# Kernel tuning notes

Measured on AMD Instinct MI355X. Metric: run time of the kernel, lower is better.

Reference implementation:

```python
import jax, jax.numpy as jnp
import numpy as np

N_NODES = 50000
N_EDGES = 800000
NEG_SLOPE = 0.2


def gat_conv(x, W, al, ar, b, src, dst, num_nodes):
    # x: [N, Din]; W: [Din, H*Dout]; al/ar: [H, Dout]; b: [H*Dout]
    H, Dout = al.shape
    h = (x @ W).reshape(num_nodes, H, Dout)            # [N, H, Dout]
    el = jnp.sum(h * al[None], axis=-1)                # [N, H]
    er = jnp.sum(h * ar[None], axis=-1)                # [N, H]
    e = jax.nn.leaky_relu(el[src] + er[dst], NEG_SLOPE)  # [E, H]
    # segment softmax over incoming edges of each dst node
    m = jax.ops.segment_max(e, dst, num_segments=num_nodes)
    m = jnp.where(jnp.isfinite(m), m, 0.0)
    ex = jnp.exp(e - m[dst])                           # [E, H]
    s = jax.ops.segment_sum(ex, dst, num_segments=num_nodes)
    alpha = ex / s[dst]                                # [E, H]
    msg = h[src] * alpha[:, :, None]                   # [E, H, Dout]
    out = jax.ops.segment_sum(msg, dst, num_segments=num_nodes)
    return out + b.reshape(1, H, Dout)                 # [N, H, Dout]


def setup_inputs() -> dict:
    key = jax.random.key(0)
    ks = jax.random.split(key, 12)
    d_in, hid, heads = 128, 128, 2
    inp = {
        "embedding": jax.random.normal(ks[0], (N_NODES, d_in), jnp.float32),
        "W0": jax.random.normal(ks[1], (d_in, heads * hid), jnp.float32) * 0.1,
        "al0": jax.random.normal(ks[2], (heads, hid), jnp.float32) * 0.1,
        "ar0": jax.random.normal(ks[3], (heads, hid), jnp.float32) * 0.1,
        "b0": jnp.zeros((heads * hid,), jnp.float32),
        "W1": jax.random.normal(ks[4], (heads * hid, heads * hid), jnp.float32) * 0.1,
        "al1": jax.random.normal(ks[5], (1, heads * hid), jnp.float32) * 0.1,
        "ar1": jax.random.normal(ks[6], (1, heads * hid), jnp.float32) * 0.1,
        "b1": jnp.zeros((heads * hid,), jnp.float32),
        "src": jax.random.randint(ks[7], (N_EDGES,), 0, N_NODES, jnp.int32),
        "dst": jax.random.randint(ks[8], (N_EDGES,), 0, N_NODES, jnp.int32),
    }
    return inp


def reference(embedding, W0, al0, ar0, b0, W1, al1, ar1, b1, src, dst):
    n = embedding.shape[0]
    # layer 0: 2 heads, then flatten heads and ReLU (dropout no-op in eval)
    x = gat_conv(embedding, W0, al0, ar0, b0, src, dst, n)  # [N, 2, 128]
    x = jax.nn.relu(x.reshape(n, -1))                        # [N, 256]
    # layer 1: 1 head, squeeze
    x = gat_conv(x, W1, al1, ar1, b1, src, dst, n)           # [N, 1, 256]
    x = x.reshape(n, -1)
    x = x.at[0].set(0.0)
    return x
```

## Files before the change

kernel.cpp:

```cpp
#include <hip/hip_runtime.h>


typedef __attribute__((ext_vector_type(8))) short short8v;
typedef __attribute__((ext_vector_type(4))) float f32x4;

#define LOG2E 1.4426950408889634f

__device__ inline unsigned short f2bf(float x) {
    union { float f; unsigned int u; } v; v.f = x;
    unsigned int r = v.u + 0x7fffu + ((v.u >> 16) & 1u);
    return (unsigned short)(r >> 16);
}
__device__ inline float bf2f(unsigned short h) {
    union { unsigned int u; float f; } v; v.u = ((unsigned int)h) << 16;
    return v.f;
}

__global__ void convW_both(const float* __restrict__ W0, unsigned short* __restrict__ W0t,
                           const float* __restrict__ W1, unsigned short* __restrict__ W1t)
{
    int t = blockIdx.x * blockDim.x + threadIdx.x;
    if (t < 128 * 256) {
        int k = t >> 8, n2 = t & 255;
        W0t[n2 * 128 + k] = f2bf(W0[t]);
    }
    int u = t - 128 * 256;
    if (u >= 0 && u < 256 * 256) {
        int k = u >> 8, n2 = u & 255;
        W1t[n2 * 256 + k] = f2bf(W1[u]);
    }
}

template<int AFP32, int H>
__global__ __launch_bounds__(256) void gemm_fused(
    const void* __restrict__ Av, const unsigned short* __restrict__ Bt,
    unsigned short* __restrict__ C,
    const float* __restrict__ al, const float* __restrict__ ar,
    float* __restrict__ el, float* __restrict__ er,
    int M, int N, int K)
{
    __shared__ __align__(16) unsigned short As[128 * 64];
    __shared__ __align__(16) unsigned short Bs[64 * 64];
    const int tid = threadIdx.x;
    const int lane = tid & 63, wv = tid >> 6;
    const int rowBase = blockIdx.x * 128;
    const int colBase = blockIdx.y * 64;

    f32x4 acc[2][4];
    #pragma unroll
    for (int i = 0; i < 2; ++i)
        #pragma unroll
        for (int j = 0; j < 4; ++j)
            acc[i][j] = (f32x4){0.f, 0.f, 0.f, 0.f};

    for (int k0 = 0; k0 < K; k0 += 64) {
        #pragma unroll
        for (int c = tid; c < 128 * 8; c += 256) {
            int row = c >> 3, cc = c & 7;
            int gr = rowBase + row; if (gr >= M) gr = M - 1;
            unsigned short* dstp = &As[row * 64 + (cc ^ (row & 7)) * 8];
            if (AFP32) {
                const float* A = (const float*)Av;
                const float* ap = A + (size_t)gr * K + k0 + cc * 8;
                float4 v0 = *(const float4*)ap;
                float4 v1 = *(const float4*)(ap + 4);
                ushort4 o0, o1;
                o0.x = f2bf(v0.x); o0.y = f2bf(v0.y); o0.z = f2bf(v0.z); o0.w = f2bf(v0.w);
                o1.x = f2bf(v1.x); o1.y = f2bf(v1.y); o1.z = f2bf(v1.z); o1.w = f2bf(v1.w);
                *(ushort4*)dstp = o0;
                *(ushort4*)(dstp + 4) = o1;
            } else {
                const unsigned short* A = (const unsigned short*)Av;
                int4 v = *(const int4*)(A + (size_t)gr * K + k0 + cc * 8);
                *(int4*)dstp = v;
            }
        }
        #pragma unroll
        for (int c = tid; c < 64 * 8; c += 256) {
            int n2 = c >> 3, cc = c & 7;
            int4 v = *(const int4*)(Bt + (size_t)(colBase + n2) * K + k0 + cc * 8);
            *(int4*)&Bs[n2 * 64 + (cc ^ (n2 & 7)) * 8] = v;
        }
        __syncthreads();

        #pragma unroll
        for (int ks = 0; ks < 64; ks += 32) {
            int kchunk = (ks >> 3) + (lane >> 4);
            short8v af[2], bfr[4];
            #pragma unroll
            for (int fm = 0; fm < 2; ++fm) {
                int ml = wv * 32 + fm * 16 + (lane & 15);
                af[fm] = *(const short8v*)&As[ml * 64 + (kchunk ^ (ml & 7)) * 8];
            }
            #pragma unroll
            for (int fi = 0; fi < 4; ++fi) {
                int nl = fi * 16 + (lane & 15);
                bfr[fi] = *(const short8v*)&Bs[nl * 64 + (kchunk ^ (nl & 7)) * 8];
            }
            #pragma unroll
            for (int fm = 0; fm < 2; ++fm)
                #pragma unroll
                for (int fi = 0; fi < 4; ++fi)
                    acc[fm][fi] = __builtin_amdgcn_mfma_f32_16x16x32_bf16(
                        af[fm], bfr[fi], acc[fm][fi], 0, 0, 0);
        }
        __syncthreads();
    }

    float alv[4], arv[4];
    #pragma unroll
    for (int fi = 0; fi < 4; ++fi) {
        int col = colBase + fi * 16 + (lane & 15);
        alv[fi] = al[col];
        arv[fi] = ar[col];
    }
    const int head = (H == 2) ? (colBase >> 7) : 0;

    #pragma unroll
    for (int fm = 0; fm < 2; ++fm) {
        #pragma unroll
        for (int r = 0; r < 4; ++r) {
            int row = rowBase + wv * 32 + fm * 16 + (lane >> 4) * 4 + r;
            float pe = acc[fm][0][r] * alv[0] + acc[fm][1][r] * alv[1]
                     + acc[fm][2][r] * alv[2] + acc[fm][3][r] * alv[3];
            float pr2 = acc[fm][0][r] * arv[0] + acc[fm][1][r] * arv[1]
                      + acc[fm][2][r] * arv[2] + acc[fm][3][r] * arv[3];
            #pragma unroll
            for (int off = 8; off; off >>= 1) {
                pe  += __shfl_xor(pe, off);
                pr2 += __shfl_xor(pr2, off);
            }
            if (row < M) {
                #pragma unroll
                for (int fi = 0; fi < 4; ++fi) {
                    int col = colBase + fi * 16 + (lane & 15);
                    C[(size_t)row * N + col] = f2bf(acc[fm][fi][r]);
                }
                if ((lane & 15) == 0) {
                    atomicAdd(&el[row * H + head], pe);
                    atomicAdd(&er[row * H + head], pr2);
                }
            }
        }
    }
}

__global__ void count_kernel(const int* __restrict__ dst, int* __restrict__ cnt, int E)
{
    int t = blockIdx.x * blockDim.x + threadIdx.x;
    if (t < E) atomicAdd(&cnt[dst[t]], 1);
}

__global__ __launch_bounds__(256) void scan_partial(const int* __restrict__ cnt,
                                                    int* __restrict__ bsum, int n)
{
    int t = threadIdx.x;
    int idx = blockIdx.x * 1024 + t * 4;
    int4 v = make_int4(0, 0, 0, 0);
    if (idx + 3 < n) v = *(const int4*)(cnt + idx);
    else if (idx < n) {
        v.x = cnt[idx];
        if (idx + 1 < n) v.y = cnt[idx + 1];
        if (idx + 2 < n) v.z = cnt[idx + 2];
    }
    int s = v.x + v.y + v.z + v.w;
    #pragma unroll
    for (int off = 32; off; off >>= 1) s += __shfl_xor(s, off);
    __shared__ int ws[4];
    if ((t & 63) == 0) ws[t >> 6] = s;
    __syncthreads();
    if (t == 0) bsum[blockIdx.x] = ws[0] + ws[1] + ws[2] + ws[3];
}

__global__ void scan_bsum(int* __restrict__ bsum, int* __restrict__ row,
                          int nb, int n, int E)
{
    int t = threadIdx.x;
    if (nb <= 64) {
        int v = (t < nb) ? bsum[t] : 0;
        int x = v;
        #pragma unroll
        for (int off = 1; off < 64; off <<= 1) {
            int y = __shfl_up(x, off);
            if (t >= off) x += y;
        }
        if (t < nb) bsum[t] = x - v;
    } else if (t == 0) {
        int run = 0;
        for (int i = 0; i < nb; ++i) { int v = bsum[i]; bsum[i] = run; run += v; }
    }
    if (t == 0) row[n] = E;
}

__global__ __launch_bounds__(256) void scan_final(
    const int* __restrict__ cnt, const int* __restrict__ bsum,
    int* __restrict__ row, int* __restrict__ cursor, int n)
{
    int t = threadIdx.x;
    int lane = t & 63;
    int idx = blockIdx.x * 1024 + t * 4;
    int4 v = make_int4(0, 0, 0, 0);
    if (idx + 3 < n) v = *(const int4*)(cnt + idx);
    else if (idx < n) {
        v.x = cnt[idx];
        if (idx + 1 < n) v.y = cnt[idx + 1];
        if (idx + 2 < n) v.z = cnt[idx + 2];
    }
    int s1 = v.x + v.y, s2 = s1 + v.z, s3 = s2 + v.w;
    int tsum = s3;
    int x = tsum;
    #pragma unroll
    for (int off = 1; off < 64; off <<= 1) {
        int y = __shfl_up(x, off);
        if (lane >= off) x += y;
    }
    int wex = x - tsum;
    __shared__ int ws[4];
    if (lane == 63) ws[t >> 6] = x;
    __syncthreads();
    int off0 = bsum[blockIdx.x];
    for (int w2 = 0; w2 < (t >> 6); ++w2) off0 += ws[w2];
    int e0 = off0 + wex;
    if (idx < n)     { row[idx]     = e0;        cursor[idx]     = e0; }
    if (idx + 1 < n) { row[idx + 1] = e0 + v.x;  cursor[idx + 1] = e0 + v.x; }
    if (idx + 2 < n) { row[idx + 2] = e0 + s1;   cursor[idx + 2] = e0 + s1; }
    if (idx + 3 < n) { row[idx + 3] = e0 + s2;   cursor[idx + 3] = e0 + s2; }
}

__global__ void fill_kernel(const int* __restrict__ src, const int* __restrict__ dst,
                            int* __restrict__ cursor, int* __restrict__ srcc, int E)
{
    int t = blockIdx.x * blockDim.x + threadIdx.x;
    if (t < E) {
        int pos = atomicAdd(&cursor[dst[t]], 1);
        srcc[pos] = src[t];
    }
}

template<int H>
__global__ __launch_bounds__(256) void agg_kernel(
    const unsigned short* __restrict__ h, const float* __restrict__ el,
    const float* __restrict__ er, float* __restrict__ ecsr,
    const int* __restrict__ srcc, const int* __restrict__ row,
    const float* __restrict__ bias, float* __restrict__ outf,
    unsigned short* __restrict__ outb, int n_nodes, int E,
    int do_relu, int zero0)
{
    int wid = blockIdx.x * 4 + (threadIdx.x >> 6);
    if (wid >= n_nodes) return;
    int lane = threadIdx.x & 63;
    int beg = __builtin_amdgcn_readfirstlane(row[wid]);
    int end = __builtin_amdgcn_readfirstlane(row[wid + 1]);
    const int hsel   = (H == 2) ? (lane >> 5) : 0;
    const int stride = (H == 2) ? 32 : 64;
    const int l0     = (H == 2) ? (lane & 31) : lane;
    float* plane = ecsr + (size_t)hsel * E;
    const float rr = er[wid * H + hsel];

    float m = -1e30f, s = 0.f;
    for (int i = beg + l0; i < end; i += stride) {
        int sn = srcc[i];
        float v = el[sn * H + hsel] + rr;
        float ev = ((v > 0.f) ? v : 0.2f * v) * LOG2E;
        plane[i] = ev;
        float mn = fmaxf(m, ev);
        s = s * exp2f(m - mn) + exp2f(ev - mn);
        m = mn;
    }
    #pragma unroll
    for (int off = (H == 2) ? 16 : 32; off; off >>= 1) {
        float mo = __shfl_xor(m, off);
        float so = __shfl_xor(s, off);
        float mn = fmaxf(m, mo);
        s = s * exp2f(m - mn) + so * exp2f(mo - mn);
        m = mn;
    }
    float r = (s > 0.f) ? 1.f / s : 0.f;
    __threadfence_block();

    float aA0 = 0.f, aA1 = 0.f, aA2 = 0.f, aA3 = 0.f;
    float aB0 = 0.f, aB1 = 0.f, aB2 = 0.f, aB3 = 0.f;
    float aC0 = 0.f, aC1 = 0.f, aC2 = 0.f, aC3 = 0.f;
    float aD0 = 0.f, aD1 = 0.f, aD2 = 0.f, aD3 = 0.f;
    int i = beg;
    for (; i + 3 < end; i += 4) {
        float wa = exp2f(plane[i]     - m);
        float wb = exp2f(plane[i + 1] - m);
        float wc = exp2f(plane[i + 2] - m);
        float wd = exp2f(plane[i + 3] - m);
        int sa = srcc[i], sb = srcc[i + 1], sc2 = srcc[i + 2], sd = srcc[i + 3];
        ushort4 ha = *(const ushort4*)(h + (size_t)sa * 256 + lane * 4);
        ushort4 hb = *(const ushort4*)(h + (size_t)sb * 256 + lane * 4);
        ushort4 hc = *(const ushort4*)(h + (size_t)sc2 * 256 + lane * 4);
        ushort4 hd = *(const ushort4*)(h + (size_t)sd * 256 + lane * 4);
        aA0 = fmaf(wa, bf2f(ha.x), aA0); aB0 = fmaf(wb, bf2f(hb.x), aB0);
        aC0 = fmaf(wc, bf2f(hc.x), aC0); aD0 = fmaf(wd, bf2f(hd.x), aD0);
        aA1 = fmaf(wa, bf2f(ha.y), aA1); aB1 = fmaf(wb, bf2f(hb.y), aB1);
        aC1 = fmaf(wc, bf2f(hc.y), aC1); aD1 = fmaf(wd, bf2f(hd.y), aD1);
        aA2 = fmaf(wa, bf2f(ha.z), aA2); aB2 = fmaf(wb, bf2f(hb.z), aB2);
        aC2 = fmaf(wc, bf2f(hc.z), aC2); aD2 = fmaf(wd, bf2f(hd.z), aD2);
        aA3 = fmaf(wa, bf2f(ha.w), aA3); aB3 = fmaf(wb, bf2f(hb.w), aB3);
        aC3 = fmaf(wc, bf2f(hc.w), aC3); aD3 = fmaf(wd, bf2f(hd.w), aD3);
    }
    for (; i < end; ++i) {
        float wa = exp2f(plane[i] - m);
        int sa = srcc[i];
        ushort4 ha = *(const ushort4*)(h + (size_t)sa * 256 + lane * 4);
        aA0 = fmaf(wa, bf2f(ha.x), aA0);
        aA1 = fmaf(wa, bf2f(ha.y), aA1);
        aA2 = fmaf(wa, bf2f(ha.z), aA2);
        aA3 = fmaf(wa, bf2f(ha.w), aA3);
    }

    float4 b4 = *(const float4*)(bias + lane * 4);
    float o0 = ((aA0 + aB0) + (aC0 + aD0)) * r + b4.x;
    float o1 = ((aA1 + aB1) + (aC1 + aD1)) * r + b4.y;
    float o2 = ((aA2 + aB2) + (aC2 + aD2)) * r + b4.z;
    float o3 = ((aA3 + aB3) + (aC3 + aD3)) * r + b4.w;
    if (do_relu) {
        o0 = fmaxf(o0, 0.f); o1 = fmaxf(o1, 0.f);
        o2 = fmaxf(o2, 0.f); o3 = fmaxf(o3, 0.f);
    }
    if (zero0 && wid == 0) { o0 = o1 = o2 = o3 = 0.f; }
    size_t base = (size_t)wid * 256 + lane * 4;
    if (outb) {
        ushort4 o; o.x = f2bf(o0); o.y = f2bf(o1); o.z = f2bf(o2); o.w = f2bf(o3);
        *(ushort4*)(outb + base) = o;
    } else {
        *(float4*)(outf + base) = make_float4(o0, o1, o2, o3);
    }
}

extern "C" void kernel_launch(void* const* d_in, const int* in_sizes, int n_in,
                              void* d_out, int out_size, void* d_ws, size_t ws_size,
                              hipStream_t stream)
{
    const float* emb = (const float*)d_in[0];
    const float* W0  = (const float*)d_in[1];
    const float* al0 = (const float*)d_in[2];
    const float* ar0 = (const float*)d_in[3];
    const float* b0  = (const float*)d_in[4];
    const float* W1  = (const float*)d_in[5];
    const float* al1 = (const float*)d_in[6];
    const float* ar1 = (const float*)d_in[7];
    const float* b1  = (const float*)d_in[8];
    const int* src   = (const int*)d_in[9];
    const int* dst   = (const int*)d_in[10];
    const int N = in_sizes[0] / 128;
    const int E = in_sizes[9];
    float* outp = (float*)d_out;

    char* w = (char*)d_ws;
    auto alloc = [&](size_t bytes) {
        char* p = w;
        w += (bytes + 255) & ~(size_t)255;
        return p;
    };
    unsigned short* hb  = (unsigned short*)alloc((size_t)N * 256 * 2);
    unsigned short* x1b = (unsigned short*)alloc((size_t)N * 256 * 2);
    float* ecsr = (float*)alloc((size_t)E * 2 * 4);
    int* srcc   = (int*)alloc((size_t)E * 4);
    int* rowp   = (int*)alloc((size_t)(N + 1) * 4);
    float* el   = (float*)alloc((size_t)N * 2 * 4);
    float* er   = (float*)alloc((size_t)N * 2 * 4);
    int* cnt    = (int*)alloc((size_t)N * 4);
    int* cursor = (int*)alloc((size_t)N * 4);
    int* bsum   = (int*)alloc(1024 * 4);
    unsigned short* W0t = (unsigned short*)alloc(256 * 128 * 2);
    unsigned short* W1t = (unsigned short*)alloc(256 * 256 * 2);

    const int nbScan = (N + 1023) / 1024;

    convW_both<<<(128 * 256 + 256 * 256 + 255) / 256, 256, 0, stream>>>(
        W0, W0t, W1, W1t);

    hipMemsetAsync(cnt, 0, (size_t)N * 4, stream);
    count_kernel<<<(E + 255) / 256, 256, 0, stream>>>(dst, cnt, E);
    scan_partial<<<nbScan, 256, 0, stream>>>(cnt, bsum, N);
    scan_bsum<<<1, 64, 0, stream>>>(bsum, rowp, nbScan, N, E);
    scan_final<<<nbScan, 256, 0, stream>>>(cnt, bsum, rowp, cursor, N);
    fill_kernel<<<(E + 255) / 256, 256, 0, stream>>>(src, dst, cursor, srcc, E);

    hipMemsetAsync(el, 0, (size_t)N * 2 * 4, stream);
    hipMemsetAsync(er, 0, (size_t)N * 2 * 4, stream);
    gemm_fused<1, 2><<<dim3((N + 127) / 128, 4), 256, 0, stream>>>(
        emb, W0t, hb, al0, ar0, el, er, N, 256, 128);
    agg_kernel<2><<<(N + 3) / 4, 256, 0, stream>>>(
        hb, el, er, ecsr, srcc, rowp, b0, nullptr, x1b, N, E, 1, 0);

    hipMemsetAsync(el, 0, (size_t)N * 4, stream);
    hipMemsetAsync(er, 0, (size_t)N * 4, stream);
    gemm_fused<0, 1><<<dim3((N + 127) / 128, 4), 256, 0, stream>>>(
        x1b, W1t, hb, al1, ar1, el, er, N, 256, 256);
    agg_kernel<1><<<(N + 3) / 4, 256, 0, stream>>>(
        hb, el, er, ecsr, srcc, rowp, b1, outp, nullptr, N, E, 0, 1);
}
```

Measured before the change: 288.0 us.

## Split aggregation across two waves per node, recompute scores, fold memsets into kernels

The aggregation kernel now assigns two waves per destination node, each handling half of the 256 feature columns (one head for layer 0). Edge scores are recomputed in the accumulation loop instead of being written to and reread from an E-sized scratch buffer. The weight conversion is merged into the degree-count kernel, and the el/er zeroing memsets move into scan_final and the layer-0 aggregation kernel. This removes several launches and the scratch traffic, at the cost of duplicating the softmax-max pass in both waves and doing narrower per-lane gathers.

Result: slower. 327.6 us (+13.8%).

```diff
diff --git a/kernel.cpp b/kernel.cpp
--- a/kernel.cpp
+++ b/kernel.cpp
@@ -14,21 +14,6 @@
 __device__ inline float bf2f(unsigned short h) {
     union { unsigned int u; float f; } v; v.u = ((unsigned int)h) << 16;
     return v.f;
-}
-
-__global__ void convW_both(const float* __restrict__ W0, unsigned short* __restrict__ W0t,
-                           const float* __restrict__ W1, unsigned short* __restrict__ W1t)
-{
-    int t = blockIdx.x * blockDim.x + threadIdx.x;
-    if (t < 128 * 256) {
-        int k = t >> 8, n2 = t & 255;
-        W0t[n2 * 128 + k] = f2bf(W0[t]);
-    }
-    int u = t - 128 * 256;
-    if (u >= 0 && u < 256 * 256) {
-        int k = u >> 8, n2 = u & 255;
-        W1t[n2 * 256 + k] = f2bf(W1[u]);
-    }
 }
 
 template<int AFP32, int H>
@@ -145,10 +130,27 @@
     }
 }
 
-__global__ void count_kernel(const int* __restrict__ dst, int* __restrict__ cnt, int E)
-{
-    int t = blockIdx.x * blockDim.x + threadIdx.x;
-    if (t < E) atomicAdd(&cnt[dst[t]], 1);
+__global__ void conv_count(const float* __restrict__ W0, unsigned short* __restrict__ W0t,
+                           const float* __restrict__ W1, unsigned short* __restrict__ W1t,
+                           const int* __restrict__ dst, int* __restrict__ cnt,
+                           int nbW, int E)
+{
+    int bid = blockIdx.x;
+    if (bid < nbW) {
+        int t = bid * 256 + threadIdx.x;
+        if (t < 128 * 256) {
+            int k = t >> 8, n2 = t & 255;
+            W0t[n2 * 128 + k] = f2bf(W0[t]);
+        }
+        int u = t - 128 * 256;
+        if (u >= 0 && u < 256 * 256) {
+            int k = u >> 8, n2 = u & 255;
+            W1t[n2 * 256 + k] = f2bf(W1[u]);
+        }
+    } else {
+        int t = (bid - nbW) * 256 + threadIdx.x;
+        if (t < E) atomicAdd(&cnt[dst[t]], 1);
+    }
 }
 
 __global__ __launch_bounds__(256) void scan_partial(const int* __restrict__ cnt,
@@ -194,7 +196,8 @@
 
 __global__ __launch_bounds__(256) void scan_final(
     const int* __restrict__ cnt, const int* __restrict__ bsum,
-    int* __restrict__ row, int* __restrict__ cursor, int n)
+    int* __restrict__ row, int* __restrict__ cursor,
+    float* __restrict__ el0, float* __restrict__ er0, int n)
 {
     int t = threadIdx.x;
     int lane = t & 63;
@@ -221,10 +224,15 @@
     int off0 = bsum[blockIdx.x];
     for (int w2 = 0; w2 < (t >> 6); ++w2) off0 += ws[w2];
     int e0 = off0 + wex;
-    if (idx < n)     { row[idx]     = e0;        cursor[idx]     = e0; }
-    if (idx + 1 < n) { row[idx + 1] = e0 + v.x;  cursor[idx + 1] = e0 + v.x; }
-    if (idx + 2 < n) { row[idx + 2] = e0 + s1;   cursor[idx + 2] = e0 + s1; }
-    if (idx + 3 < n) { row[idx + 3] = e0 + s2;   cursor[idx + 3] = e0 + s2; }
+    float2 z2 = make_float2(0.f, 0.f);
+    if (idx < n)     { row[idx]     = e0;        cursor[idx]     = e0;
+                       *(float2*)(el0 + 2*idx)     = z2; *(float2*)(er0 + 2*idx)     = z2; }
+    if (idx + 1 < n) { row[idx + 1] = e0 + v.x;  cursor[idx + 1] = e0 + v.x;
+                       *(float2*)(el0 + 2*idx + 2) = z2; *(float2*)(er0 + 2*idx + 2) = z2; }
+    if (idx + 2 < n) { row[idx + 2] = e0 + s1;   cursor[idx + 2] = e0 + s1;
+                       *(float2*)(el0 + 2*idx + 4) = z2; *(float2*)(er0 + 2*idx + 4) = z2; }
+    if (idx + 3 < n) { row[idx + 3] = e0 + s2;   cursor[idx + 3] = e0 + s2;
+                       *(float2*)(el0 + 2*idx + 6) = z2; *(float2*)(er0 + 2*idx + 6) = z2; }
 }
 
 __global__ void fill_kernel(const int* __restrict__ src, const int* __restrict__ dst,
@@ -240,35 +248,35 @@
 template<int H>
 __global__ __launch_bounds__(256) void agg_kernel(
     const unsigned short* __restrict__ h, const float* __restrict__ el,
-    const float* __restrict__ er, float* __restrict__ ecsr,
-    const int* __restrict__ srcc, const int* __restrict__ row,
-    const float* __restrict__ bias, float* __restrict__ outf,
-    unsigned short* __restrict__ outb, int n_nodes, int E,
-    int do_relu, int zero0)
-{
-    int wid = blockIdx.x * 4 + (threadIdx.x >> 6);
+    const float* __restrict__ er, const int* __restrict__ srcc,
+    const int* __restrict__ row, const float* __restrict__ bias,
+    float* __restrict__ outf, unsigned short* __restrict__ outb,
+    float* __restrict__ elz, float* __restrict__ erz,
+    int n_nodes, int do_relu, int zero0)
+{
+    int gw = blockIdx.x * 4 + (threadIdx.x >> 6);
+    int wid = gw >> 1, half = gw & 1;
     if (wid >= n_nodes) return;
     int lane = threadIdx.x & 63;
     int beg = __builtin_amdgcn_readfirstlane(row[wid]);
     int end = __builtin_amdgcn_readfirstlane(row[wid + 1]);
-    const int hsel   = (H == 2) ? (lane >> 5) : 0;
-    const int stride = (H == 2) ? 32 : 64;
-    const int l0     = (H == 2) ? (lane & 31) : lane;
-    float* plane = ecsr + (size_t)hsel * E;
-    const float rr = er[wid * H + hsel];
+    const int head = (H == 2) ? half : 0;
+    const float rr = er[wid * H + head];
+
+    if (elz && lane == 0) {
+        if (half == 0) elz[wid] = 0.f; else erz[wid] = 0.f;
+    }
 
     float m = -1e30f, s = 0.f;
-    for (int i = beg + l0; i < end; i += stride) {
-        int sn = srcc[i];
-        float v = el[sn * H + hsel] + rr;
+    for (int i = beg + lane; i < end; i += 64) {
+        float v = el[srcc[i] * H + head] + rr;
         float ev = ((v > 0.f) ? v : 0.2f * v) * LOG2E;
-        plane[i] = ev;
         float mn = fmaxf(m, ev);
         s = s * exp2f(m - mn) + exp2f(ev - mn);
         m = mn;
     }
     #pragma unroll
-    for (int off = (H == 2) ? 16 : 32; off; off >>= 1) {
+    for (int off = 32; off; off >>= 1) {
         float mo = __shfl_xor(m, off);
         float so = __shfl_xor(s, off);
         float mn = fmaxf(m, mo);
@@ -276,58 +284,49 @@
         m = mn;
     }
     float r = (s > 0.f) ? 1.f / s : 0.f;
-    __threadfence_block();
-
-    float aA0 = 0.f, aA1 = 0.f, aA2 = 0.f, aA3 = 0.f;
-    float aB0 = 0.f, aB1 = 0.f, aB2 = 0.f, aB3 = 0.f;
-    float aC0 = 0.f, aC1 = 0.f, aC2 = 0.f, aC3 = 0.f;
-    float aD0 = 0.f, aD1 = 0.f, aD2 = 0.f, aD3 = 0.f;
+
+    const int cb = half * 128 + lane * 2;
+    float a0 = 0.f, a1 = 0.f, b0 = 0.f, b1 = 0.f;
+    float c0 = 0.f, c1 = 0.f, d0 = 0.f, d1 = 0.f;
     int i = beg;
     for (; i + 3 < end; i += 4) {
-        float wa = exp2f(plane[i]     - m);
-        float wb = exp2f(plane[i + 1] - m);
-        float wc = exp2f(plane[i + 2] - m);
-        float wd = exp2f(plane[i + 3] - m);
-        int sa = srcc[i], sb = srcc[i + 1], sc2 = srcc[i + 2], sd = srcc[i + 3];
-        ushort4 ha = *(const ushort4*)(h + (size_t)sa * 256 + lane * 4);
-        ushort4 hb = *(const ushort4*)(h + (size_t)sb * 256 + lane * 4);
-        ushort4 hc = *(const ushort4*)(h + (size_t)sc2 * 256 + lane * 4);
-        ushort4 hd = *(const ushort4*)(h + (size_t)sd * 256 + lane * 4);
-        aA0 = fmaf(wa, bf2f(ha.x), aA0); aB0 = fmaf(wb, bf2f(hb.x), aB0);
-        aC0 = fmaf(wc, bf2f(hc.x), aC0); aD0 = fmaf(wd, bf2f(hd.x), aD0);
-        aA1 = fmaf(wa, bf2f(ha.y), aA1); aB1 = fmaf(wb, bf2f(hb.y), aB1);
-        aC1 = fmaf(wc, bf2f(hc.y), aC1); aD1 = fmaf(wd, bf2f(hd.y), aD1);
-        aA2 = fmaf(wa, bf2f(ha.z), aA2); aB2 = fmaf(wb, bf2f(hb.z), aB2);
-        aC2 = fmaf(wc, bf2f(hc.z), aC2); aD2 = fmaf(wd, bf2f(hd.z), aD2);
-        aA3 = fmaf(wa, bf2f(ha.w), aA3); aB3 = fmaf(wb, bf2f(hb.w), aB3);
-        aC3 = fmaf(wc, bf2f(hc.w), aC3); aD3 = fmaf(wd, bf2f(hd.w), aD3);
+        int sa = srcc[i], sb = srcc[i + 1], sc = srcc[i + 2], sd = srcc[i + 3];
+        float va = el[sa * H + head] + rr;
+        float vb = el[sb * H + head] + rr;
+        float vc = el[sc * H + head] + rr;
+        float vd = el[sd * H + head] + rr;
+        float wa = exp2f(((va > 0.f) ? va : 0.2f * va) * LOG2E - m);
+        float wb = exp2f(((vb > 0.f) ? vb : 0.2f * vb) * LOG2E - m);
+        float wc = exp2f(((vc > 0.f) ? vc : 0.2f * vc) * LOG2E - m);
+        float wd = exp2f(((vd > 0.f) ? vd : 0.2f * vd) * LOG2E - m);
+        ushort2 ha = *(const ushort2*)(h + (size_t)sa * 256 + cb);
+        ushort2 hb = *(const ushort2*)(h + (size_t)sb * 256 + cb);
+        ushort2 hc = *(const ushort2*)(h + (size_t)sc * 256 + cb);
+        ushort2 hd = *(const ushort2*)(h + (size_t)sd * 256 + cb);
+        a0 = fmaf(wa, bf2f(ha.x), a0); a1 = fmaf(wa, bf2f(ha.y), a1);
+        b0 = fmaf(wb, bf2f(hb.x), b0); b1 = fmaf(wb, bf2f(hb.y), b1);
+        c0 = fmaf(wc, bf2f(hc.x), c0); c1 = fmaf(wc, bf2f(hc.y), c1);
+        d0 = fmaf(wd, bf2f(hd.x), d0); d1 = fmaf(wd, bf2f(hd.y), d1);
     }
     for (; i < end; ++i) {
-        float wa = exp2f(plane[i] - m);
         int sa = srcc[i];
-        ushort4 ha = *(const ushort4*)(h + (size_t)sa * 256 + lane * 4);
-        aA0 = fmaf(wa, bf2f(ha.x), aA0);
-        aA1 = fmaf(wa, bf2f(ha.y), aA1);
-        aA2 = fmaf(wa, bf2f(ha.z), aA2);
-        aA3 = fmaf(wa, bf2f(ha.w), aA3);
-    }
-
-    float4 b4 = *(const float4*)(bias + lane * 4);
-    float o0 = ((aA0 + aB0) + (aC0 + aD0)) * r + b4.x;
-    float o1 = ((aA1 + aB1) + (aC1 + aD1)) * r + b4.y;
-    float o2 = ((aA2 + aB2) + (aC2 + aD2)) * r + b4.z;
-    float o3 = ((aA3 + aB3) + (aC3 + aD3)) * r + b4.w;
-    if (do_relu) {
-        o0 = fmaxf(o0, 0.f); o1 = fmaxf(o1, 0.f);
-        o2 = fmaxf(o2, 0.f); o3 = fmaxf(o3, 0.f);
-    }
-    if (zero0 && wid == 0) { o0 = o1 = o2 = o3 = 0.f; }
-    size_t base = (size_t)wid * 256 + lane * 4;
+        float va = el[sa * H + head] + rr;
+        float wa = exp2f(((va > 0.f) ? va : 0.2f * va) * LOG2E - m);
+        ushort2 ha = *(const ushort2*)(h + (size_t)sa * 256 + cb);
+        a0 = fmaf(wa, bf2f(ha.x), a0); a1 = fmaf(wa, bf2f(ha.y), a1);
+    }
+
+    float2 b2 = *(const float2*)(bias + cb);
+    float o0 = ((a0 + b0) + (c0 + d0)) * r + b2.x;
+    float o1 = ((a1 + b1) + (c1 + d1)) * r + b2.y;
+    if (do_relu) { o0 = fmaxf(o0, 0.f); o1 = fmaxf(o1, 0.f); }
+    if (zero0 && wid == 0) { o0 = o1 = 0.f; }
+    size_t base = (size_t)wid * 256 + cb;
     if (outb) {
-        ushort4 o; o.x = f2bf(o0); o.y = f2bf(o1); o.z = f2bf(o2); o.w = f2bf(o3);
-        *(ushort4*)(outb + base) = o;
+        ushort2 o; o.x = f2bf(o0); o.y = f2bf(o1);
+        *(ushort2*)(outb + base) = o;
     } else {
-        *(float4*)(outf + base) = make_float4(o0, o1, o2, o3);
+        *(float2*)(outf + base) = make_float2(o0, o1);
     }
 }
 
@@ -358,11 +357,12 @@
     };
     unsigned short* hb  = (unsigned short*)alloc((size_t)N * 256 * 2);
     unsigned short* x1b = (unsigned short*)alloc((size_t)N * 256 * 2);
-    float* ecsr = (float*)alloc((size_t)E * 2 * 4);
     int* srcc   = (int*)alloc((size_t)E * 4);
     int* rowp   = (int*)alloc((size_t)(N + 1) * 4);
-    float* el   = (float*)alloc((size_t)N * 2 * 4);
-    float* er   = (float*)alloc((size_t)N * 2 * 4);
+    float* el0  = (float*)alloc((size_t)N * 2 * 4);
+    float* er0  = (float*)alloc((size_t)N * 2 * 4);
+    float* el1  = (float*)alloc((size_t)N * 4);
+    float* er1  = (float*)alloc((size_t)N * 4);
     int* cnt    = (int*)alloc((size_t)N * 4);
     int* cursor = (int*)alloc((size_t)N * 4);
     int* bsum   = (int*)alloc(1024 * 4);
@@ -370,28 +370,23 @@
     unsigned short* W1t = (unsigned short*)alloc(256 * 256 * 2);
 
     const int nbScan = (N + 1023) / 1024;
-
-    convW_both<<<(128 * 256 + 256 * 256 + 255) / 256, 256, 0, stream>>>(
-        W0, W0t, W1, W1t);
+    const int nbW = (128 * 256 + 256 * 256 + 255) / 256;
 
     hipMemsetAsync(cnt, 0, (size_t)N * 4, stream);
-    count_kernel<<<(E + 255) / 256, 256, 0, stream>>>(dst, cnt, E);
+    conv_count<<<nbW + (E + 255) / 256, 256, 0, stream>>>(
+        W0, W0t, W1, W1t, dst, cnt, nbW, E);
     scan_partial<<<nbScan, 256, 0, stream>>>(cnt, bsum, N);
     scan_bsum<<<1, 64, 0, stream>>>(bsum, rowp, nbScan, N, E);
-    scan_final<<<nbScan, 256, 0, stream>>>(cnt, bsum, rowp, cursor, N);
+    scan_final<<<nbScan, 256, 0, stream>>>(cnt, bsum, rowp, cursor, el0, er0, N);
     fill_kernel<<<(E + 255) / 256, 256, 0, stream>>>(src, dst, cursor, srcc, E);
 
-    hipMemsetAsync(el, 0, (size_t)N * 2 * 4, stream);
-    hipMemsetAsync(er, 0, (size_t)N * 2 * 4, stream);
     gemm_fused<1, 2><<<dim3((N + 127) / 128, 4), 256, 0, stream>>>(
-        emb, W0t, hb, al0, ar0, el, er, N, 256, 128);
-    agg_kernel<2><<<(N + 3) / 4, 256, 0, stream>>>(
-        hb, el, er, ecsr, srcc, rowp, b0, nullptr, x1b, N, E, 1, 0);
-
-    hipMemsetAsync(el, 0, (size_t)N * 4, stream);
-    hipMemsetAsync(er, 0, (size_t)N * 4, stream);
+        emb, W0t, hb, al0, ar0, el0, er0, N, 256, 128);
+    agg_kernel<2><<<(2 * N + 3) / 4, 256, 0, stream>>>(
+        hb, el0, er0, srcc, rowp, b0, nullptr, x1b, el1, er1, N, 1, 0);
+
     gemm_fused<0, 1><<<dim3((N + 127) / 128, 4), 256, 0, stream>>>(
-        x1b, W1t, hb, al1, ar1, el, er, N, 256, 256);
-    agg_kernel<1><<<(N + 3) / 4, 256, 0, stream>>>(
-        hb, el, er, ecsr, srcc, rowp, b1, outp, nullptr, N, E, 0, 1);
-}
+        x1b, W1t, hb, al1, ar1, el1, er1, N, 256, 256);
+    agg_kernel<1><<<(2 * N + 3) / 4, 256, 0, stream>>>(
+        hb, el1, er1, srcc, rowp, b1, outp, nullptr, nullptr, nullptr, N, 0, 1);
+}
```
